# Kernel optimization log

Measured on AMD Instinct MI355X. Metric: run time of the kernel, lower is better.

## Reference

```python
import jax, jax.numpy as jnp
import numpy as np

EMBED_DIM = 1024
NUM_HEADS = 16
HEAD_DIM = EMBED_DIM // NUM_HEADS


def setup_inputs() -> dict:
    key = jax.random.key(0)
    ks = jax.random.split(key, 9)
    B, S, D = 4, 2048, EMBED_DIM
    scale = 1.0 / np.sqrt(D)
    inp = {
        "x": jax.random.normal(ks[0], (B, S, D), dtype=jnp.float32),
        "wq": jax.random.normal(ks[1], (D, D), dtype=jnp.float32) * scale,
        "bq": jnp.zeros((D,), dtype=jnp.float32),
        "wk": jax.random.normal(ks[2], (D, D), dtype=jnp.float32) * scale,
        "bk": jnp.zeros((D,), dtype=jnp.float32),
        "wv": jax.random.normal(ks[3], (D, D), dtype=jnp.float32) * scale,
        "bv": jnp.zeros((D,), dtype=jnp.float32),
        "wo": jax.random.normal(ks[4], (D, D), dtype=jnp.float32) * scale,
        "bo": jnp.zeros((D,), dtype=jnp.float32),
    }
    return inp


def reference(x, wq, bq, wk, bk, wv, bv, wo, bo):
    B, S, D = x.shape
    H, Hd = NUM_HEADS, HEAD_DIM

    def split_heads(t):
        # [B, S, D] -> [B, H, S, Hd]
        return t.reshape(B, S, H, Hd).transpose(0, 2, 1, 3)

    q = split_heads(x @ wq.T + bq)
    k = split_heads(x @ wk.T + bk)
    v = split_heads(x @ wv.T + bv)

    scores = jnp.einsum("bhqd,bhkd->bhqk", q, k) / jnp.sqrt(jnp.float32(Hd))
    attn = jax.nn.softmax(scores, axis=-1)
    out = jnp.einsum("bhqk,bhkd->bhqd", attn, v)  # [B, H, S, Hd]
    out = out.transpose(0, 2, 1, 3).reshape(B, S, D)
    return out @ wo.T + bo
```

## Files before the change

kernel.cpp:

```cpp
#include <hip/hip_runtime.h>
#include <hip/hip_bf16.h>
#include <hip/hip_fp16.h>

typedef _Float16 f16;
typedef f16 f16x8 __attribute__((ext_vector_type(8)));
typedef f16 f16x4 __attribute__((ext_vector_type(4)));
typedef f16 f16x2 __attribute__((ext_vector_type(2)));
typedef float f32x4 __attribute__((ext_vector_type(4)));
typedef float f32x16 __attribute__((ext_vector_type(16)));
typedef unsigned int u32x4 __attribute__((ext_vector_type(4)));
typedef unsigned int u32x2 __attribute__((ext_vector_type(2)));

#define MFMA16(a, b, c) __builtin_amdgcn_mfma_f32_16x16x32_f16(a, b, c, 0, 0, 0)
#define MFMA32(a, b, c) __builtin_amdgcn_mfma_f32_32x32x16_f16(a, b, c, 0, 0, 0)

constexpr int BB = 4, SS = 2048, DD = 1024, HH = 16, HDIM = 64;
constexpr int MM = BB * SS;
constexpr float QSCALE = 0.125f * 1.44269504088896340736f;


__device__ __forceinline__ void gl_lds16(const void* g, void* l) {
  __builtin_amdgcn_global_load_lds((const __attribute__((address_space(1))) void*)g,
                                   (__attribute__((address_space(3))) void*)l, 16, 0, 0);
}

__global__ __launch_bounds__(256) void cvt_all_kernel(const float* __restrict__ x,
                                                      const float* __restrict__ w0,
                                                      const float* __restrict__ w1,
                                                      const float* __restrict__ w2,
                                                      const float* __restrict__ w3,
                                                      f16* xh, f16* o0, f16* o1,
                                                      f16* o2, f16* o3) {
  int bid = blockIdx.x;
  const float* in; f16* out; int idx;
  if (bid < MM * DD / 4 / 256) {
    in = x; out = xh; idx = bid * 256 + threadIdx.x;
  } else {
    int wb = bid - MM * DD / 4 / 256;
    int which = wb >> 10;
    in = which == 0 ? w0 : which == 1 ? w1 : which == 2 ? w2 : w3;
    out = which == 0 ? o0 : which == 1 ? o1 : which == 2 ? o2 : o3;
    idx = (wb & 1023) * 256 + threadIdx.x;
  }
  f32x4 v = reinterpret_cast<const f32x4*>(in)[idx];
  f16x4 o;
  o[0] = (f16)v[0]; o[1] = (f16)v[1]; o[2] = (f16)v[2]; o[3] = (f16)v[3];
  reinterpret_cast<f16x4*>(out)[idx] = o;
}

__device__ __forceinline__ int swz(int row, int slot) {
  return row * 64 + ((slot ^ (row & 7)) << 3);
}

__global__ __launch_bounds__(256) void qkv_kernel(const f16* __restrict__ A,
                                                  const f16* __restrict__ Wq,
                                                  const f16* __restrict__ Wk,
                                                  const f16* __restrict__ Wv,
                                                  const float* __restrict__ bq,
                                                  const float* __restrict__ bk,
                                                  const float* __restrict__ bv,
                                                  f16* __restrict__ Qo,
                                                  f16* __restrict__ Ko,
                                                  f16* __restrict__ Vo) {
  constexpr int K = 1024;
  __shared__ __align__(16) char smem_raw[128 * 136 * 2];
  f16* As = (f16*)smem_raw;
  f16* Ws = As + 128 * 64;

  const int p = blockIdx.x;
  const int bx = (p >> 3) % 24;
  const int by = (p & 7) + 8 * ((p >> 3) / 24);

  const int mat = bx >> 3;
  const f16* W = mat == 0 ? Wq : (mat == 1 ? Wk : Wv);
  const float* bias = mat == 0 ? bq : (mat == 1 ? bk : bv);
  const float scale = mat == 0 ? QSCALE : 1.0f;

  const int tid = threadIdx.x;
  const int m0 = by * 128, n0 = (bx & 7) * 128;
  const int w = tid >> 6, lane = tid & 63;
  const int wm = (w >> 1) * 64, wn = (w & 1) * 64;
  const int g = lane >> 4, r = lane & 15;
  const int srow = lane >> 3;
  const int sslot = (lane & 7) ^ srow;

  f32x4 acc[4][4] = {};

  for (int k0 = 0; k0 < K; k0 += 64) {
#pragma unroll
    for (int i = 0; i < 4; ++i) {
      int rbase = w * 32 + i * 8;
      gl_lds16(A + (size_t)(m0 + rbase + srow) * K + k0 + sslot * 8, As + rbase * 64);
      gl_lds16(W + (size_t)(n0 + rbase + srow) * K + k0 + sslot * 8, Ws + rbase * 64);
    }
    __syncthreads();

#pragma unroll
    for (int ks = 0; ks < 2; ++ks) {
      f16x8 af[4], bf[4];
#pragma unroll
      for (int i = 0; i < 4; ++i) {
        af[i] = *reinterpret_cast<const f16x8*>(As + swz(wm + i * 16 + r, (ks << 2) | g));
        bf[i] = *reinterpret_cast<const f16x8*>(Ws + swz(wn + i * 16 + r, (ks << 2) | g));
      }
#pragma unroll
      for (int i = 0; i < 4; ++i)
#pragma unroll
        for (int j = 0; j < 4; ++j)
          acc[i][j] = MFMA16(af[i], bf[j], acc[i][j]);
    }
    __syncthreads();
  }

  if (mat == 0) {
#pragma unroll
    for (int i = 0; i < 4; ++i)
#pragma unroll
      for (int j = 0; j < 4; ++j)
#pragma unroll
        for (int q = 0; q < 4; ++q) {
          int gm = m0 + wm + i * 16 + g * 4 + q;
          int gn = n0 + wn + j * 16 + r;
          float v = (acc[i][j][q] + bias[gn]) * scale;
          int b = gm >> 11, s = gm & 2047;
          int h = gn >> 6, hd = gn & 63;
          Qo[(((size_t)(b * HH + h)) * SS + s) * HDIM + hd] = (f16)v;
        }
  } else if (mat == 1) {
#pragma unroll
    for (int i = 0; i < 4; ++i)
#pragma unroll
      for (int j = 0; j < 4; ++j)
#pragma unroll
        for (int q = 0; q < 4; ++q) {
          int gm = m0 + wm + i * 16 + g * 4 + q;
          int gn = n0 + wn + j * 16 + r;
          float v = acc[i][j][q] + bias[gn];
          int b = gm >> 11, s = gm & 2047;
          int h = gn >> 6, hd = gn & 63;
          int tile = s >> 6, row = s & 63, slot = hd >> 3, w8 = hd & 7;
          size_t off = ((((size_t)(b * HH + h) * 32 + tile) * 8 + slot) * 64 + row) * 8 + w8;
          Ko[off] = (f16)v;
        }
  } else {
    __syncthreads();
    f16* T = (f16*)smem_raw;
#pragma unroll
    for (int i = 0; i < 4; ++i)
#pragma unroll
      for (int j = 0; j < 4; ++j)
#pragma unroll
        for (int q = 0; q < 4; ++q) {
          int ml = wm + i * 16 + g * 4 + q;
          int nl = wn + j * 16 + r;
          T[nl * 136 + ml] = (f16)(acc[i][j][q] + bias[n0 + nl]);
        }
    __syncthreads();
    const int b = m0 >> 11, sbase = m0 & 2047;
#pragma unroll
    for (int it = 0; it < 8; ++it) {
      int cid = it * 256 + tid;
      int hd_l = cid & 127, sl = (cid >> 7) & 7, tl = cid >> 10;
      u32x4 v = *reinterpret_cast<const u32x4*>(T + hd_l * 136 + tl * 64 + sl * 8);
      int gn = n0 + hd_l, h = gn >> 6, hd = gn & 63;
      int tile = (sbase >> 6) + tl;
      size_t off = ((((size_t)(b * HH + h) * 32 + tile) * 8 + sl) * 64 + hd) * 8;
      *reinterpret_cast<u32x4*>(Vo + off) = v;
    }
  }
}

__global__ __launch_bounds__(256) void oproj_kernel(const f16* __restrict__ A,
                                                    const f16* __restrict__ W,
                                                    const float* __restrict__ bias,
                                                    float* __restrict__ Out) {
  constexpr int K = 1024, N = 1024;
  __shared__ __align__(16) f16 As[128 * 64];
  __shared__ __align__(16) f16 Ws[128 * 64];

  const int p = blockIdx.x;
  const int bx = (p >> 3) & 7;
  const int by = (p & 7) | ((p >> 6) << 3);

  const int tid = threadIdx.x;
  const int m0 = by * 128, n0 = bx * 128;
  const int w = tid >> 6, lane = tid & 63;
  const int wm = (w >> 1) * 64, wn = (w & 1) * 64;
  const int g = lane >> 4, r = lane & 15;
  const int srow = lane >> 3;
  const int sslot = (lane & 7) ^ srow;

  f32x4 acc[4][4] = {};

  for (int k0 = 0; k0 < K; k0 += 64) {
#pragma unroll
    for (int i = 0; i < 4; ++i) {
      int rbase = w * 32 + i * 8;
      gl_lds16(A + (size_t)(m0 + rbase + srow) * K + k0 + sslot * 8, As + rbase * 64);
      gl_lds16(W + (size_t)(n0 + rbase + srow) * K + k0 + sslot * 8, Ws + rbase * 64);
    }
    __syncthreads();

#pragma unroll
    for (int ks = 0; ks < 2; ++ks) {
      f16x8 af[4], bf[4];
#pragma unroll
      for (int i = 0; i < 4; ++i) {
        af[i] = *reinterpret_cast<const f16x8*>(As + swz(wm + i * 16 + r, (ks << 2) | g));
        bf[i] = *reinterpret_cast<const f16x8*>(Ws + swz(wn + i * 16 + r, (ks << 2) | g));
      }
#pragma unroll
      for (int i = 0; i < 4; ++i)
#pragma unroll
        for (int j = 0; j < 4; ++j)
          acc[i][j] = MFMA16(af[i], bf[j], acc[i][j]);
    }
    __syncthreads();
  }

#pragma unroll
  for (int i = 0; i < 4; ++i)
#pragma unroll
    for (int j = 0; j < 4; ++j)
#pragma unroll
      for (int q = 0; q < 4; ++q) {
        int gm = m0 + wm + i * 16 + g * 4 + q;
        int gn = n0 + wn + j * 16 + r;
        Out[(size_t)gm * N + gn] = acc[i][j][q] + bias[gn];
      }
}

__global__ __launch_bounds__(256, 2) void attn_kernel(const f16* __restrict__ Q,
                                                      const f16* __restrict__ K,
                                                      const f16* __restrict__ Vt,
                                                      f16* __restrict__ AO) {
  __shared__ __align__(16) f16 Kls[2][8 * 512];
  __shared__ __align__(16) f16 Vls[2][8 * 512];
  __shared__ __align__(16) float Lw[4][64];

  const int p = blockIdx.x;
  const int qx = (p >> 3) & 7;
  const int bh = (p & 7) | ((p >> 6) << 3);
  const int q0 = qx * 256;

  const int tid = threadIdx.x;
  const int w = tid >> 6, lane = tid & 63;
  const int q31 = lane & 31;
  const int h = lane >> 5;
  const f16* Kg = K + (size_t)bh * (SS * HDIM);
  const f16* Vg = Vt + (size_t)bh * (SS * HDIM);
  const int s0 = 2 * w;
  const int rofs = h * 512 + q31 * 8;

  const f16* Qg = Q + ((size_t)bh * SS + q0 + w * 64 + q31) * HDIM + 8 * h;
  f16x8 qf[2][4];
#pragma unroll
  for (int f = 0; f < 2; ++f)
#pragma unroll
    for (int m = 0; m < 4; ++m)
      qf[f][m] = *reinterpret_cast<const f16x8*>(Qg + f * 32 * HDIM + 16 * m);

  f32x16 oacc[2][2] = {};
  float lsum0 = 0.f, lsum1 = 0.f;

#pragma unroll
  for (int i = 0; i < 2; ++i) {
    int s_idx = s0 + i;
    gl_lds16(Kg + (size_t)(s_idx * 64 + lane) * 8, &Kls[0][s_idx * 512]);
    gl_lds16(Vg + (size_t)(s_idx * 64 + lane) * 8, &Vls[0][s_idx * 512]);
  }
  __syncthreads();

  for (int t = 0; t < SS / 64; ++t) {
    const int cur = t & 1;
    if (t < SS / 64 - 1) {
#pragma unroll
      for (int i = 0; i < 2; ++i) {
        int s_idx = s0 + i;
        gl_lds16(Kg + (size_t)((t + 1) * 512 + s_idx * 64 + lane) * 8,
                 &Kls[cur ^ 1][s_idx * 512]);
        gl_lds16(Vg + (size_t)((t + 1) * 512 + s_idx * 64 + lane) * 8,
                 &Vls[cur ^ 1][s_idx * 512]);
      }
    }
    const f16* Kc = &Kls[cur][0];
    const f16* Vc = &Vls[cur][0];

#pragma unroll
    for (int kb = 0; kb < 2; ++kb) {
      f32x16 sc0 = {}, sc1 = {};
      __builtin_amdgcn_s_setprio(1);
#pragma unroll
      for (int m = 0; m < 4; ++m) {
        f16x8 kf = *reinterpret_cast<const f16x8*>(Kc + m * 1024 + kb * 256 + rofs);
        sc0 = MFMA32(kf, qf[0][m], sc0);
        sc1 = MFMA32(kf, qf[1][m], sc1);
      }
      __builtin_amdgcn_s_setprio(0);

      unsigned pk0[8], pk1[8];
#pragma unroll
      for (int rp = 0; rp < 4; ++rp)
#pragma unroll
        for (int pp = 0; pp < 2; ++pp) {
          float a0 = __builtin_amdgcn_exp2f(sc0[4 * rp + 2 * pp]);
          float a1 = __builtin_amdgcn_exp2f(sc0[4 * rp + 2 * pp + 1]);
          pk0[2 * rp + pp] = __builtin_bit_cast(unsigned, __builtin_amdgcn_cvt_pkrtz(a0, a1));
          float b0 = __builtin_amdgcn_exp2f(sc1[4 * rp + 2 * pp]);
          float b1 = __builtin_amdgcn_exp2f(sc1[4 * rp + 2 * pp + 1]);
          pk1[2 * rp + pp] = __builtin_bit_cast(unsigned, __builtin_amdgcn_cvt_pkrtz(b0, b1));
        }

      {
        f16x2 s01 = __builtin_bit_cast(f16x2, pk0[0]) + __builtin_bit_cast(f16x2, pk0[1]);
        f16x2 s23 = __builtin_bit_cast(f16x2, pk0[2]) + __builtin_bit_cast(f16x2, pk0[3]);
        f16x2 s45 = __builtin_bit_cast(f16x2, pk0[4]) + __builtin_bit_cast(f16x2, pk0[5]);
        f16x2 s67 = __builtin_bit_cast(f16x2, pk0[6]) + __builtin_bit_cast(f16x2, pk0[7]);
        f16x2 st = (s01 + s23) + (s45 + s67);
        lsum0 += (float)st[0] + (float)st[1];
      }
      {
        f16x2 s01 = __builtin_bit_cast(f16x2, pk1[0]) + __builtin_bit_cast(f16x2, pk1[1]);
        f16x2 s23 = __builtin_bit_cast(f16x2, pk1[2]) + __builtin_bit_cast(f16x2, pk1[3]);
        f16x2 s45 = __builtin_bit_cast(f16x2, pk1[4]) + __builtin_bit_cast(f16x2, pk1[5]);
        f16x2 s67 = __builtin_bit_cast(f16x2, pk1[6]) + __builtin_bit_cast(f16x2, pk1[7]);
        f16x2 st = (s01 + s23) + (s45 + s67);
        lsum1 += (float)st[0] + (float)st[1];
      }

#pragma unroll
      for (int jl = 0; jl < 2; ++jl) {
        auto a0 = __builtin_amdgcn_permlane32_swap(pk0[4 * jl + 0], pk0[4 * jl + 2], false, false);
        auto a1 = __builtin_amdgcn_permlane32_swap(pk0[4 * jl + 1], pk0[4 * jl + 3], false, false);
        u32x4 fa = {(unsigned)a0[0], (unsigned)a1[0], (unsigned)a0[1], (unsigned)a1[1]};
        f16x8 pa0 = __builtin_bit_cast(f16x8, fa);
        auto b0 = __builtin_amdgcn_permlane32_swap(pk1[4 * jl + 0], pk1[4 * jl + 2], false, false);
        auto b1 = __builtin_amdgcn_permlane32_swap(pk1[4 * jl + 1], pk1[4 * jl + 3], false, false);
        u32x4 fb = {(unsigned)b0[0], (unsigned)b1[0], (unsigned)b0[1], (unsigned)b1[1]};
        f16x8 pa1 = __builtin_bit_cast(f16x8, fb);
        const int j = 2 * kb + jl;
        __builtin_amdgcn_s_setprio(1);
#pragma unroll
        for (int vb = 0; vb < 2; ++vb) {
          f16x8 vbf = *reinterpret_cast<const f16x8*>(Vc + j * 1024 + vb * 256 + rofs);
          oacc[0][vb] = MFMA32(pa0, vbf, oacc[0][vb]);
          oacc[1][vb] = MFMA32(pa1, vbf, oacc[1][vb]);
        }
        __builtin_amdgcn_s_setprio(0);
      }
    }
    __syncthreads();
  }

  lsum0 += __shfl_xor(lsum0, 32, 64);
  lsum1 += __shfl_xor(lsum1, 32, 64);
  if (h == 0) {
    Lw[w][q31] = 1.0f / lsum0;
    Lw[w][32 + q31] = 1.0f / lsum1;
  }

  const int b = bh >> 4, head = bh & 15;
#pragma unroll
  for (int f = 0; f < 2; ++f) {
    f32x4 li[4];
#pragma unroll
    for (int rq = 0; rq < 4; ++rq)
      li[rq] = *reinterpret_cast<const f32x4*>(&Lw[w][32 * f + 8 * rq + 4 * h]);
    f16* aobase = AO + ((size_t)(b * SS + q0 + 64 * w + 32 * f)) * DD + head * 64 + q31;
#pragma unroll
    for (int vb = 0; vb < 2; ++vb)
#pragma unroll
      for (int reg = 0; reg < 16; ++reg) {
        int q = (reg & 3) + 8 * (reg >> 2) + 4 * h;
        aobase[(size_t)q * DD + 32 * vb] = (f16)(oacc[f][vb][reg] * li[reg >> 2][reg & 3]);
      }
  }
}

extern "C" void kernel_launch(void* const* d_in, const int* in_sizes, int n_in,
                              void* d_out, int out_size, void* d_ws, size_t ws_size,
                              hipStream_t stream) {
  (void)in_sizes; (void)n_in; (void)out_size; (void)ws_size;
  const float* x  = (const float*)d_in[0];
  const float* wq = (const float*)d_in[1];
  const float* bq = (const float*)d_in[2];
  const float* wk = (const float*)d_in[3];
  const float* bk = (const float*)d_in[4];
  const float* wv = (const float*)d_in[5];
  const float* bv = (const float*)d_in[6];
  const float* wo = (const float*)d_in[7];
  const float* bo = (const float*)d_in[8];
  float* out = (float*)d_out;

  char* ws = (char*)d_ws;
  f16* xh  = (f16*)ws; ws += (size_t)MM * DD * 2;
  f16* wqh = (f16*)ws; ws += (size_t)DD * DD * 2;
  f16* wkh = (f16*)ws; ws += (size_t)DD * DD * 2;
  f16* wvh = (f16*)ws; ws += (size_t)DD * DD * 2;
  f16* woh = (f16*)ws; ws += (size_t)DD * DD * 2;
  f16* Qb  = (f16*)ws; ws += (size_t)MM * DD * 2;
  f16* Kb  = (f16*)ws; ws += (size_t)MM * DD * 2;
  f16* Vtb = (f16*)ws; ws += (size_t)MM * DD * 2;
  f16* AOb = (f16*)ws; ws += (size_t)MM * DD * 2;

  cvt_all_kernel<<<MM * DD / 4 / 256 + 4 * (DD * DD / 4 / 256), 256, 0, stream>>>(
      x, wq, wk, wv, wo, xh, wqh, wkh, wvh, woh);

  qkv_kernel<<<1536, 256, 0, stream>>>(xh, wqh, wkh, wvh, bq, bk, bv, Qb, Kb, Vtb);

  attn_kernel<<<512, 256, 0, stream>>>(Qb, Kb, Vtb, AOb);

  oproj_kernel<<<512, 256, 0, stream>>>(AOb, woh, bo, out);
}
```

Before: 189.6 us.

## Software-pipeline attention PV with next QK and stage K epilogue via LDS

In the attention kernel, each half-tile's PV matmul is deferred so it is issued alongside the next half-tile's QK matmul. This interleaves the MFMA work with the exp/softmax work so the matrix units stay busy. V gets a third LDS buffer so the deferred PV can still read the previous tile's data while the next tile is prefetched. Separately, the QKV projection's K epilogue now goes through a padded LDS transpose tile (stride 152) with 16-byte vector stores, replacing scattered 2-byte global writes. Both add LDS usage and register pressure, which may reduce occupancy.

Result: faster. 179.7 us (-5.2%).

```diff
diff --git a/kernel.cpp b/kernel.cpp
--- a/kernel.cpp
+++ b/kernel.cpp
@@ -63,7 +63,8 @@
                                                   f16* __restrict__ Ko,
                                                   f16* __restrict__ Vo) {
   constexpr int K = 1024;
-  __shared__ __align__(16) char smem_raw[128 * 136 * 2];
+  constexpr int TS = 152;
+  __shared__ __align__(16) char smem_raw[128 * TS * 2];
   f16* As = (f16*)smem_raw;
   f16* Ws = As + 128 * 64;
 
@@ -127,22 +128,6 @@
           Qo[(((size_t)(b * HH + h)) * SS + s) * HDIM + hd] = (f16)v;
         }
   } else if (mat == 1) {
-#pragma unroll
-    for (int i = 0; i < 4; ++i)
-#pragma unroll
-      for (int j = 0; j < 4; ++j)
-#pragma unroll
-        for (int q = 0; q < 4; ++q) {
-          int gm = m0 + wm + i * 16 + g * 4 + q;
-          int gn = n0 + wn + j * 16 + r;
-          float v = acc[i][j][q] + bias[gn];
-          int b = gm >> 11, s = gm & 2047;
-          int h = gn >> 6, hd = gn & 63;
-          int tile = s >> 6, row = s & 63, slot = hd >> 3, w8 = hd & 7;
-          size_t off = ((((size_t)(b * HH + h) * 32 + tile) * 8 + slot) * 64 + row) * 8 + w8;
-          Ko[off] = (f16)v;
-        }
-  } else {
     __syncthreads();
     f16* T = (f16*)smem_raw;
 #pragma unroll
@@ -153,7 +138,33 @@
         for (int q = 0; q < 4; ++q) {
           int ml = wm + i * 16 + g * 4 + q;
           int nl = wn + j * 16 + r;
-          T[nl * 136 + ml] = (f16)(acc[i][j][q] + bias[n0 + nl]);
+          T[ml * TS + nl] = (f16)(acc[i][j][q] + bias[n0 + nl]);
+        }
+    __syncthreads();
+    const int b = m0 >> 11, sbase = m0 & 2047;
+#pragma unroll
+    for (int it = 0; it < 8; ++it) {
+      int cid = it * 256 + tid;
+      int row_s = cid & 127, ns = cid >> 7;
+      u32x4 v = *reinterpret_cast<const u32x4*>(T + row_s * TS + ns * 8);
+      int gn0 = n0 + ns * 8;
+      int h = gn0 >> 6, slot = (gn0 & 63) >> 3;
+      int tile = (sbase >> 6) + (row_s >> 6), row = row_s & 63;
+      size_t off = ((((size_t)(b * HH + h) * 32 + tile) * 8 + slot) * 64 + row) * 8;
+      *reinterpret_cast<u32x4*>(Ko + off) = v;
+    }
+  } else {
+    __syncthreads();
+    f16* T = (f16*)smem_raw;
+#pragma unroll
+    for (int i = 0; i < 4; ++i)
+#pragma unroll
+      for (int j = 0; j < 4; ++j)
+#pragma unroll
+        for (int q = 0; q < 4; ++q) {
+          int ml = wm + i * 16 + g * 4 + q;
+          int nl = wn + j * 16 + r;
+          T[nl * TS + ml] = (f16)(acc[i][j][q] + bias[n0 + nl]);
         }
     __syncthreads();
     const int b = m0 >> 11, sbase = m0 & 2047;
@@ -161,7 +172,7 @@
     for (int it = 0; it < 8; ++it) {
       int cid = it * 256 + tid;
       int hd_l = cid & 127, sl = (cid >> 7) & 7, tl = cid >> 10;
-      u32x4 v = *reinterpret_cast<const u32x4*>(T + hd_l * 136 + tl * 64 + sl * 8);
+      u32x4 v = *reinterpret_cast<const u32x4*>(T + hd_l * TS + tl * 64 + sl * 8);
       int gn = n0 + hd_l, h = gn >> 6, hd = gn & 63;
       int tile = (sbase >> 6) + tl;
       size_t off = ((((size_t)(b * HH + h) * 32 + tile) * 8 + sl) * 64 + hd) * 8;
@@ -235,7 +246,7 @@
                                                       const f16* __restrict__ Vt,
                                                       f16* __restrict__ AO) {
   __shared__ __align__(16) f16 Kls[2][8 * 512];
-  __shared__ __align__(16) f16 Vls[2][8 * 512];
+  __shared__ __align__(16) f16 Vls[3][8 * 512];
   __shared__ __align__(16) float Lw[4][64];
 
   const int p = blockIdx.x;
@@ -262,6 +273,7 @@
 
   f32x16 oacc[2][2] = {};
   float lsum0 = 0.f, lsum1 = 0.f;
+  unsigned pkP0[8], pkP1[8];
 
 #pragma unroll
   for (int i = 0; i < 2; ++i) {
@@ -271,85 +283,107 @@
   }
   __syncthreads();
 
+#define QK_PHASE(KC, KB, SC0, SC1)                                                   \
+  do {                                                                               \
+    _Pragma("unroll") for (int m = 0; m < 4; ++m) {                                  \
+      f16x8 kf = *reinterpret_cast<const f16x8*>((KC) + m * 1024 + (KB)*256 + rofs); \
+      SC0 = MFMA32(kf, qf[0][m], SC0);                                               \
+      SC1 = MFMA32(kf, qf[1][m], SC1);                                               \
+    }                                                                                \
+  } while (0)
+
+#define PV_PHASE(VPTR, JB)                                                               \
+  do {                                                                                   \
+    _Pragma("unroll") for (int jl = 0; jl < 2; ++jl) {                                   \
+      auto a0 = __builtin_amdgcn_permlane32_swap(pkP0[4 * jl + 0], pkP0[4 * jl + 2],     \
+                                                 false, false);                          \
+      auto a1 = __builtin_amdgcn_permlane32_swap(pkP0[4 * jl + 1], pkP0[4 * jl + 3],     \
+                                                 false, false);                          \
+      u32x4 fa = {(unsigned)a0[0], (unsigned)a1[0], (unsigned)a0[1], (unsigned)a1[1]};   \
+      f16x8 pa0 = __builtin_bit_cast(f16x8, fa);                                         \
+      auto b0 = __builtin_amdgcn_permlane32_swap(pkP1[4 * jl + 0], pkP1[4 * jl + 2],     \
+                                                 false, false);                          \
+      auto b1 = __builtin_amdgcn_permlane32_swap(pkP1[4 * jl + 1], pkP1[4 * jl + 3],     \
+                                                 false, false);                          \
+      u32x4 fb = {(unsigned)b0[0], (unsigned)b1[0], (unsigned)b0[1], (unsigned)b1[1]};   \
+      f16x8 pa1 = __builtin_bit_cast(f16x8, fb);                                         \
+      const int j = (JB) + jl;                                                           \
+      _Pragma("unroll") for (int vb = 0; vb < 2; ++vb) {                                 \
+        f16x8 vbf = *reinterpret_cast<const f16x8*>((VPTR) + j * 1024 + vb * 256 + rofs);\
+        oacc[0][vb] = MFMA32(pa0, vbf, oacc[0][vb]);                                     \
+        oacc[1][vb] = MFMA32(pa1, vbf, oacc[1][vb]);                                     \
+      }                                                                                  \
+    }                                                                                    \
+  } while (0)
+
+#define SM_PHASE(SC0, SC1)                                                               \
+  do {                                                                                   \
+    _Pragma("unroll") for (int rp = 0; rp < 4; ++rp)                                     \
+        _Pragma("unroll") for (int pp = 0; pp < 2; ++pp) {                               \
+      float a0 = __builtin_amdgcn_exp2f((SC0)[4 * rp + 2 * pp]);                         \
+      float a1 = __builtin_amdgcn_exp2f((SC0)[4 * rp + 2 * pp + 1]);                     \
+      pkP0[2 * rp + pp] = __builtin_bit_cast(unsigned, __builtin_amdgcn_cvt_pkrtz(a0, a1));\
+      float b0 = __builtin_amdgcn_exp2f((SC1)[4 * rp + 2 * pp]);                         \
+      float b1 = __builtin_amdgcn_exp2f((SC1)[4 * rp + 2 * pp + 1]);                     \
+      pkP1[2 * rp + pp] = __builtin_bit_cast(unsigned, __builtin_amdgcn_cvt_pkrtz(b0, b1));\
+    }                                                                                    \
+    {                                                                                    \
+      f16x2 u01 = __builtin_bit_cast(f16x2, pkP0[0]) + __builtin_bit_cast(f16x2, pkP0[1]);\
+      f16x2 u23 = __builtin_bit_cast(f16x2, pkP0[2]) + __builtin_bit_cast(f16x2, pkP0[3]);\
+      f16x2 u45 = __builtin_bit_cast(f16x2, pkP0[4]) + __builtin_bit_cast(f16x2, pkP0[5]);\
+      f16x2 u67 = __builtin_bit_cast(f16x2, pkP0[6]) + __builtin_bit_cast(f16x2, pkP0[7]);\
+      f16x2 ut = (u01 + u23) + (u45 + u67);                                              \
+      lsum0 += (float)ut[0] + (float)ut[1];                                              \
+    }                                                                                    \
+    {                                                                                    \
+      f16x2 u01 = __builtin_bit_cast(f16x2, pkP1[0]) + __builtin_bit_cast(f16x2, pkP1[1]);\
+      f16x2 u23 = __builtin_bit_cast(f16x2, pkP1[2]) + __builtin_bit_cast(f16x2, pkP1[3]);\
+      f16x2 u45 = __builtin_bit_cast(f16x2, pkP1[4]) + __builtin_bit_cast(f16x2, pkP1[5]);\
+      f16x2 u67 = __builtin_bit_cast(f16x2, pkP1[6]) + __builtin_bit_cast(f16x2, pkP1[7]);\
+      f16x2 ut = (u01 + u23) + (u45 + u67);                                              \
+      lsum1 += (float)ut[0] + (float)ut[1];                                              \
+    }                                                                                    \
+  } while (0)
+
   for (int t = 0; t < SS / 64; ++t) {
-    const int cur = t & 1;
     if (t < SS / 64 - 1) {
+      f16* kdst = &Kls[(t + 1) & 1][0];
+      f16* vdst = &Vls[(t + 1) % 3][0];
 #pragma unroll
       for (int i = 0; i < 2; ++i) {
         int s_idx = s0 + i;
-        gl_lds16(Kg + (size_t)((t + 1) * 512 + s_idx * 64 + lane) * 8,
-                 &Kls[cur ^ 1][s_idx * 512]);
-        gl_lds16(Vg + (size_t)((t + 1) * 512 + s_idx * 64 + lane) * 8,
-                 &Vls[cur ^ 1][s_idx * 512]);
+        gl_lds16(Kg + (size_t)((t + 1) * 512 + s_idx * 64 + lane) * 8, kdst + s_idx * 512);
+        gl_lds16(Vg + (size_t)((t + 1) * 512 + s_idx * 64 + lane) * 8, vdst + s_idx * 512);
       }
     }
-    const f16* Kc = &Kls[cur][0];
-    const f16* Vc = &Vls[cur][0];
-
-#pragma unroll
-    for (int kb = 0; kb < 2; ++kb) {
+    const f16* Kc = &Kls[t & 1][0];
+    const f16* Vcur = &Vls[t % 3][0];
+    const f16* Vprev = &Vls[(t + 2) % 3][0];
+
+    {
       f32x16 sc0 = {}, sc1 = {};
       __builtin_amdgcn_s_setprio(1);
-#pragma unroll
-      for (int m = 0; m < 4; ++m) {
-        f16x8 kf = *reinterpret_cast<const f16x8*>(Kc + m * 1024 + kb * 256 + rofs);
-        sc0 = MFMA32(kf, qf[0][m], sc0);
-        sc1 = MFMA32(kf, qf[1][m], sc1);
-      }
+      QK_PHASE(Kc, 0, sc0, sc1);
+      if (t > 0) PV_PHASE(Vprev, 2);
       __builtin_amdgcn_s_setprio(0);
-
-      unsigned pk0[8], pk1[8];
-#pragma unroll
-      for (int rp = 0; rp < 4; ++rp)
-#pragma unroll
-        for (int pp = 0; pp < 2; ++pp) {
-          float a0 = __builtin_amdgcn_exp2f(sc0[4 * rp + 2 * pp]);
-          float a1 = __builtin_amdgcn_exp2f(sc0[4 * rp + 2 * pp + 1]);
-          pk0[2 * rp + pp] = __builtin_bit_cast(unsigned, __builtin_amdgcn_cvt_pkrtz(a0, a1));
-          float b0 = __builtin_amdgcn_exp2f(sc1[4 * rp + 2 * pp]);
-          float b1 = __builtin_amdgcn_exp2f(sc1[4 * rp + 2 * pp + 1]);
-          pk1[2 * rp + pp] = __builtin_bit_cast(unsigned, __builtin_amdgcn_cvt_pkrtz(b0, b1));
-        }
-
-      {
-        f16x2 s01 = __builtin_bit_cast(f16x2, pk0[0]) + __builtin_bit_cast(f16x2, pk0[1]);
-        f16x2 s23 = __builtin_bit_cast(f16x2, pk0[2]) + __builtin_bit_cast(f16x2, pk0[3]);
-        f16x2 s45 = __builtin_bit_cast(f16x2, pk0[4]) + __builtin_bit_cast(f16x2, pk0[5]);
-        f16x2 s67 = __builtin_bit_cast(f16x2, pk0[6]) + __builtin_bit_cast(f16x2, pk0[7]);
-        f16x2 st = (s01 + s23) + (s45 + s67);
-        lsum0 += (float)st[0] + (float)st[1];
-      }
-      {
-        f16x2 s01 = __builtin_bit_cast(f16x2, pk1[0]) + __builtin_bit_cast(f16x2, pk1[1]);
-        f16x2 s23 = __builtin_bit_cast(f16x2, pk1[2]) + __builtin_bit_cast(f16x2, pk1[3]);
-        f16x2 s45 = __builtin_bit_cast(f16x2, pk1[4]) + __builtin_bit_cast(f16x2, pk1[5]);
-        f16x2 s67 = __builtin_bit_cast(f16x2, pk1[6]) + __builtin_bit_cast(f16x2, pk1[7]);
-        f16x2 st = (s01 + s23) + (s45 + s67);
-        lsum1 += (float)st[0] + (float)st[1];
-      }
-
-#pragma unroll
-      for (int jl = 0; jl < 2; ++jl) {
-        auto a0 = __builtin_amdgcn_permlane32_swap(pk0[4 * jl + 0], pk0[4 * jl + 2], false, false);
-        auto a1 = __builtin_amdgcn_permlane32_swap(pk0[4 * jl + 1], pk0[4 * jl + 3], false, false);
-        u32x4 fa = {(unsigned)a0[0], (unsigned)a1[0], (unsigned)a0[1], (unsigned)a1[1]};
-        f16x8 pa0 = __builtin_bit_cast(f16x8, fa);
-        auto b0 = __builtin_amdgcn_permlane32_swap(pk1[4 * jl + 0], pk1[4 * jl + 2], false, false);
-        auto b1 = __builtin_amdgcn_permlane32_swap(pk1[4 * jl + 1], pk1[4 * jl + 3], false, false);
-        u32x4 fb = {(unsigned)b0[0], (unsigned)b1[0], (unsigned)b0[1], (unsigned)b1[1]};
-        f16x8 pa1 = __builtin_bit_cast(f16x8, fb);
-        const int j = 2 * kb + jl;
-        __builtin_amdgcn_s_setprio(1);
-#pragma unroll
-        for (int vb = 0; vb < 2; ++vb) {
-          f16x8 vbf = *reinterpret_cast<const f16x8*>(Vc + j * 1024 + vb * 256 + rofs);
-          oacc[0][vb] = MFMA32(pa0, vbf, oacc[0][vb]);
-          oacc[1][vb] = MFMA32(pa1, vbf, oacc[1][vb]);
-        }
-        __builtin_amdgcn_s_setprio(0);
-      }
-    }
-    __syncthreads();
+      SM_PHASE(sc0, sc1);
+    }
+    {
+      f32x16 sc0 = {}, sc1 = {};
+      __builtin_amdgcn_s_setprio(1);
+      QK_PHASE(Kc, 1, sc0, sc1);
+      PV_PHASE(Vcur, 0);
+      __builtin_amdgcn_s_setprio(0);
+      SM_PHASE(sc0, sc1);
+    }
+    __syncthreads();
+  }
+
+  {
+    const f16* Vlast = &Vls[(SS / 64 - 1) % 3][0];
+    __builtin_amdgcn_s_setprio(1);
+    PV_PHASE(Vlast, 2);
+    __builtin_amdgcn_s_setprio(0);
   }
 
   lsum0 += __shfl_xor(lsum0, 32, 64);
@@ -375,6 +409,9 @@
         aobase[(size_t)q * DD + 32 * vb] = (f16)(oacc[f][vb][reg] * li[reg >> 2][reg & 3]);
       }
   }
+#undef QK_PHASE
+#undef PV_PHASE
+#undef SM_PHASE
 }
 
 extern "C" void kernel_launch(void* const* d_in, const int* in_sizes, int n_in,
```
